# Optimization experiments

Hardware: AMD Instinct MI355X
Metric: run time of the kernel (lower is better)

Reference implementation:

```python
import jax, jax.numpy as jnp
import numpy as np

NUM_HEADS = 8
NUM_LAYERS = 4
TOKEN_AMOUNT = 16
TOKEN_SIZE = 256
D_MODEL = 512
D_FF = 2048


def _layernorm(x, g, b, eps=1e-6):
    m = jnp.mean(x, axis=-1, keepdims=True)
    v = jnp.mean((x - m) ** 2, axis=-1, keepdims=True)
    return (x - m) / jnp.sqrt(v + eps) * g + b


def _mha(xq, xkv, W, b, mask, H):
    # W: [4, d, d] (q,k,v,o), b: [4, d]
    B, Tq, d = xq.shape
    Tk = xkv.shape[1]
    dh = d // H
    q = (xq @ W[0] + b[0]).reshape(B, Tq, H, dh).transpose(0, 2, 1, 3)
    k = (xkv @ W[1] + b[1]).reshape(B, Tk, H, dh).transpose(0, 2, 1, 3)
    v = (xkv @ W[2] + b[2]).reshape(B, Tk, H, dh).transpose(0, 2, 1, 3)
    logits = jnp.einsum('bhqd,bhkd->bhqk', q, k) / jnp.sqrt(jnp.float32(dh))
    if mask is not None:
        logits = logits - mask * jnp.finfo(jnp.float32).max
    w = jax.nn.softmax(logits, axis=-1)
    o = jnp.einsum('bhqk,bhkd->bhqd', w, v).transpose(0, 2, 1, 3).reshape(B, Tq, d)
    return o @ W[3] + b[3]


def _pos_enc(T, d):
    i = jnp.arange(d)
    factors = 1.0 / jnp.power(10000.0, (2.0 * (i // 2)).astype(jnp.float32) / d)
    ang = jnp.arange(T, dtype=jnp.float32)[:, None] * factors  # [T, d]
    return jnp.where(i % 2 == 0, jnp.sin(ang), jnp.cos(ang))


def setup_inputs() -> dict:
    key = jax.random.key(0)
    ks = jax.random.split(key, 8)
    B, Lenc, F = 16, 2048, 128
    d, dff, L, TS = D_MODEL, D_FF, NUM_LAYERS, TOKEN_SIZE
    s = 0.02
    return {
        'encoder_output': jax.random.normal(ks[0], (B, Lenc, d), jnp.float32),
        'encoder_input': jax.random.normal(ks[1], (B, Lenc, F), jnp.float32),
        'emb_W': jax.random.normal(ks[2], (TS, d), jnp.float32) * s,
        'emb_b': jnp.zeros((d,), jnp.float32),
        'out_W': jax.random.normal(ks[3], (d, TS), jnp.float32) * s,
        'out_b': jnp.zeros((TS,), jnp.float32),
        'self_W': jax.random.normal(ks[4], (L, 4, d, d), jnp.float32) * s,
        'self_b': jnp.zeros((L, 4, d), jnp.float32),
        'cross_W': jax.random.normal(ks[5], (L, 4, d, d), jnp.float32) * s,
        'cross_b': jnp.zeros((L, 4, d), jnp.float32),
        'ffn_W1': jax.random.normal(ks[6], (L, d, dff), jnp.float32) * s,
        'ffn_b1': jnp.zeros((L, dff), jnp.float32),
        'ffn_W2': jax.random.normal(ks[7], (L, dff, d), jnp.float32) * s,
        'ffn_b2': jnp.zeros((L, d), jnp.float32),
        'ln_g': jnp.ones((L, 3, d), jnp.float32),
        'ln_b': jnp.zeros((L, 3, d), jnp.float32),
    }


def reference(encoder_output, encoder_input, emb_W, emb_b, out_W, out_b,
              self_W, self_b, cross_W, cross_b,
              ffn_W1, ffn_b1, ffn_W2, ffn_b2, ln_g, ln_b):
    B = encoder_output.shape[0]
    d = emb_W.shape[1]
    H = NUM_HEADS
    # padding mask from encoder_input (mask_zero_inputs=True)
    pad_mask = jnp.min((encoder_input == 0).astype(jnp.float32), axis=2)[:, None, None, :]
    tokens = jnp.ones((B, 1, TOKEN_SIZE), dtype=jnp.float32)
    for _ in range(TOKEN_AMOUNT):
        T = tokens.shape[1]
        look_ahead = 1.0 - jnp.tril(jnp.ones((T, T), dtype=jnp.float32))
        tok_pad = jnp.min((tokens == 0).astype(jnp.float32), axis=2)[:, None, None, :]
        la_mask = jnp.maximum(tok_pad, look_ahead)
        x = (tokens @ emb_W + emb_b) * jnp.sqrt(jnp.float32(d)) + _pos_enc(T, d)
        for l in range(NUM_LAYERS):
            a = _mha(x, x, self_W[l], self_b[l], la_mask, H)
            x = _layernorm(x + a, ln_g[l, 0], ln_b[l, 0])
            c = _mha(x, encoder_output, cross_W[l], cross_b[l], pad_mask, H)
            x = _layernorm(x + c, ln_g[l, 1], ln_b[l, 1])
            f = jax.nn.relu(x @ ffn_W1[l] + ffn_b1[l]) @ ffn_W2[l] + ffn_b2[l]
            x = _layernorm(x + f, ln_g[l, 2], ln_b[l, 2])
        next_token = (x @ out_W + out_b)[:, -1:, :]
        tokens = jnp.concatenate([tokens, next_token], axis=1)
    return tokens[:, 1:, :]
```

## Files before the change

### kernel.cpp

```cpp
#include <hip/hip_runtime.h>


typedef unsigned short ushort_t;
typedef __attribute__((ext_vector_type(4))) float f32x4;
typedef __attribute__((ext_vector_type(8))) unsigned short us8;
typedef __attribute__((ext_vector_type(4))) unsigned short us4;

#define NB 256
#define NTHR 1024

__device__ __forceinline__ float bf2f(ushort_t u) {
    union { unsigned int i; float f; } v; v.i = ((unsigned int)u) << 16; return v.f;
}
__device__ __forceinline__ ushort_t f2bf(float f) {
    union { unsigned int i; float f; } v; v.f = f;
    return (ushort_t)((v.i + 0x7FFF + ((v.i >> 16) & 1)) >> 16);
}
__device__ __forceinline__ float wave_sum(float v) {
    #pragma unroll
    for (int m = 32; m; m >>= 1) v += __shfl_xor(v, m);
    return v;
}
__device__ __forceinline__ float wave_max(float v) {
    #pragma unroll
    for (int m = 32; m; m >>= 1) v = fmaxf(v, __shfl_xor(v, m));
    return v;
}

union U64C { unsigned long long u; float2 f; };
__device__ __forceinline__ float clf(const float* p) {
    return __hip_atomic_load(p, __ATOMIC_RELAXED, __HIP_MEMORY_SCOPE_AGENT);
}
__device__ __forceinline__ void csf(float* p, float v) {
    __hip_atomic_store(p, v, __ATOMIC_RELAXED, __HIP_MEMORY_SCOPE_AGENT);
}
__device__ __forceinline__ float2 clf2(const float* p) {
    U64C c; c.u = __hip_atomic_load((unsigned long long*)p, __ATOMIC_RELAXED,
                                    __HIP_MEMORY_SCOPE_AGENT);
    return c.f;
}
__device__ __forceinline__ void csf2(float* p, float x, float y) {
    U64C c; c.f.x = x; c.f.y = y;
    __hip_atomic_store((unsigned long long*)p, c.u, __ATOMIC_RELAXED,
                       __HIP_MEMORY_SCOPE_AGENT);
}

__device__ __forceinline__ void gbar(unsigned* bar, int g) {
    __syncthreads();
    if (threadIdx.x == 0) {
        unsigned* cnt = bar + g * 32;
        unsigned* rel = bar + 512 + g * 32;
        unsigned a = __hip_atomic_fetch_add(cnt, 1u, __ATOMIC_RELAXED,
                                            __HIP_MEMORY_SCOPE_AGENT);
        unsigned e = (a >> 4) + 1u;
        if ((a & 15u) == 15u) {
            __hip_atomic_store(rel, e, __ATOMIC_RELAXED, __HIP_MEMORY_SCOPE_AGENT);
        } else {
            while ((int)(__hip_atomic_load(rel, __ATOMIC_RELAXED,
                                           __HIP_MEMORY_SCOPE_AGENT) - e) < 0)
                __builtin_amdgcn_s_sleep(1);
        }
    }
    __syncthreads();
}

__device__ __forceinline__ void ln512b(const float* __restrict__ row,
                                       const float* __restrict__ g,
                                       const float* __restrict__ be,
                                       int use_ln, float* dst, float* red) {
    int tid = threadIdx.x;
    float a = (tid < 512) ? clf(row + tid) : 0.f;
    if (use_ln) {
        float s = a, s2 = a * a;
        #pragma unroll
        for (int m = 32; m; m >>= 1) {
            s  += __shfl_xor(s, m);
            s2 += __shfl_xor(s2, m);
        }
        if ((tid & 63) == 0) { red[tid >> 6] = s; red[16 + (tid >> 6)] = s2; }
        __syncthreads();
        float ts = 0.f, ts2 = 0.f;
        #pragma unroll
        for (int i = 0; i < 8; i++) { ts += red[i]; ts2 += red[16 + i]; }
        float mu = ts * (1.f / 512.f);
        float var = ts2 * (1.f / 512.f) - mu * mu;
        float rstd = rsqrtf(var + 1e-6f);
        if (tid < 512) dst[tid] = (a - mu) * rstd * g[tid] + be[tid];
    } else {
        if (tid < 512) dst[tid] = a;
    }
    __syncthreads();
}

template<int NCQ, int K>
__device__ __forceinline__ void gemv_all(const float* xs, const float* __restrict__ W,
                                         int ldw, int col0, float* part) {
    constexpr int S = 1024 / NCQ;
    constexpr int KS = K / S;
    int tid = threadIdx.x;
    int cq = tid & (NCQ - 1), ks = tid / NCQ;
    const float* Wp = W + (size_t)(ks * KS) * ldw + col0 + cq * 4;
    const float* xp = xs + ks * KS;
    f32x4 acc = {0.f, 0.f, 0.f, 0.f};
    #pragma unroll
    for (int r = 0; r < KS; r++)
        acc += xp[r] * *(const f32x4*)(Wp + (size_t)r * ldw);
    #pragma unroll
    for (int m = NCQ; m < 64; m <<= 1) {
        acc[0] += __shfl_xor(acc[0], m);
        acc[1] += __shfl_xor(acc[1], m);
        acc[2] += __shfl_xor(acc[2], m);
        acc[3] += __shfl_xor(acc[3], m);
    }
    int wave = tid >> 6, lane = tid & 63;
    if (lane < NCQ) *(f32x4*)(part + (wave * NCQ + lane) * 4) = acc;
    __syncthreads();
}
template<int NCQ>
__device__ __forceinline__ float gemv_allr(const float* part) {
    float a = 0.f;
    #pragma unroll
    for (int w = 0; w < 16; w++) a += part[w * NCQ * 4 + threadIdx.x];
    return a;
}

struct Args {
    const float *enc, *encIn, *embW, *embB, *outW, *outB;
    const float *selfW, *selfB, *crossW, *crossB;
    const float *fW1, *fb1, *fW2, *fb2, *lng, *lnb;
    float* out;
    unsigned* bar;
    float *x0, *qbuf, *y1, *y2, *y3, *attnb;
    float *lny1, *lny2, *qt, *Pm2, *Ps2, *Pz, *tmpb, *selfK, *selfV;
};


__global__ __launch_bounds__(NTHR, 4) void k_mega(Args A) {
    __shared__ ushort_t encL[128 * 520];
    __shared__ float padL[128];
    __shared__ float sm[6400];
    const int bid = blockIdx.x, tid = threadIdx.x;
    const int b = bid >> 4, r = bid & 15;
    unsigned* bar = A.bar;

    {
        const float* ep = A.enc + ((size_t)b * 2048 + r * 128) * 512;
        #pragma unroll 4
        for (int it = 0; it < 16; it++) {
            int idx = tid + it * 1024;
            int key = idx >> 7;
            int d = (idx & 127) * 4;
            float4 v = *(const float4*)(ep + (size_t)key * 512 + d);
            us4 o; o[0] = f2bf(v.x); o[1] = f2bf(v.y); o[2] = f2bf(v.z); o[3] = f2bf(v.w);
            *(us4*)(encL + key * 520 + d) = o;
        }
        int key = tid >> 3, sub = tid & 7;
        const float* p = A.encIn + ((size_t)b * 2048 + r * 128 + key) * 128 + sub * 16;
        int ok = 1;
        #pragma unroll
        for (int j = 0; j < 4; j++) {
            float4 v = *(const float4*)(p + j * 4);
            ok &= (v.x == 0.f) & (v.y == 0.f) & (v.z == 0.f) & (v.w == 0.f);
        }
        ok &= __shfl_xor(ok, 1); ok &= __shfl_xor(ok, 2); ok &= __shfl_xor(ok, 4);
        if (sub == 0) padL[key] = ok ? 1.f : 0.f;
    }
    __syncthreads();

    for (int t = 0; t < 16; t++) {
        {
            float* tok = sm;
            float* part = sm + 256;
            if (tid < 256)
                tok[tid] = (t == 0) ? 1.f
                         : clf(A.out + (size_t)b * 4096 + (t - 1) * 256 + tid);
            __syncthreads();
            gemv_all<8, 256>(tok, A.embW, 512, r * 32, part);
            if (tid < 32) {
                float acc = gemv_allr<8>(part);
                int col = r * 32 + tid;
                float expo = (2.0f * (float)(col >> 1)) * (1.f / 512.f);
                float ang = (float)t * powf(10000.0f, -expo);
                float pv = (col & 1) ? cosf(ang) : sinf(ang);
                csf(A.x0 + (size_t)b * 512 + col,
                    (acc + A.embB[col]) * 22.627416997969522f + pv);
            }
        }
        gbar(bar, b);

        for (int l = 0; l < 4; l++) {
            const float* src = (l == 0) ? A.x0 : A.y3;
            const float* gP = (l == 0) ? nullptr : A.lng + ((l - 1) * 3 + 2) * 512;
            const float* bP = (l == 0) ? nullptr : A.lnb + ((l - 1) * 3 + 2) * 512;
            int ulnP = (l != 0);

            {
                float* xs = sm;
                float* red = sm + 512;
                float* part = sm + 1024;
                ln512b(src + (size_t)b * 512, gP, bP, ulnP, xs, red);
                int cq = tid & 7, ks = tid >> 3;
                const float* xp = xs + ks * 4;
                f32x4 a0 = {0.f,0.f,0.f,0.f}, a1 = a0, a2 = a0;
                const float* W0 = A.selfW + ((size_t)(l * 4 + 0)) * 262144
                                + (size_t)(ks * 4) * 512 + r * 32 + cq * 4;
                const float* W1 = W0 + 262144;
                const float* W2 = W1 + 262144;
                #pragma unroll
                for (int rr = 0; rr < 4; rr++) {
                    float x = xp[rr];
                    a0 += x * *(const f32x4*)(W0 + (size_t)rr * 512);
                    a1 += x * *(const f32x4*)(W1 + (size_t)rr * 512);
                    a2 += x * *(const f32x4*)(W2 + (size_t)rr * 512);
                }
                #pragma unroll
                for (int m = 8; m < 64; m <<= 1) {
                    #pragma unroll
                    for (int j = 0; j < 4; j++) {
                        a0[j] += __shfl_xor(a0[j], m);
                        a1[j] += __shfl_xor(a1[j], m);
                        a2[j] += __shfl_xor(a2[j], m);
                    }
                }
                int wave = tid >> 6, lane = tid & 63;
                if (lane < 8) {
                    *(f32x4*)(part + (wave * 8 + lane) * 4) = a0;
                    *(f32x4*)(part + 512 + (wave * 8 + lane) * 4) = a1;
                    *(f32x4*)(part + 1024 + (wave * 8 + lane) * 4) = a2;
                }
                __syncthreads();
                if (tid < 96) {
                    int m = tid >> 5, j = tid & 31;
                    float a = 0.f;
                    #pragma unroll
                    for (int w = 0; w < 16; w++) a += part[m * 512 + w * 32 + j];
                    int col = r * 32 + j;
                    a += A.selfB[(l * 4 + m) * 512 + col];
                    if (m == 0) csf(A.qbuf + (size_t)b * 512 + col, a);
                    else if (m == 1)
                        csf(A.selfK + (((size_t)l * 16 + b) * 16 + t) * 512 + col, a);
                    else
                        csf(A.selfV + (((size_t)l * 16 + b) * 16 + t) * 512 + col, a);
                }
            }
            gbar(bar, b);

            {
                float* xr = sm;
                float* qs = sm + 512;
                float* as2 = sm + 1024;
                float* lg = sm + 2048;
                float* red = sm + 2176;
                float* part = sm + 2560;
                ln512b(src + (size_t)b * 512, gP, bP, ulnP, xr, red);
                if (tid < 256) {
                    float2 v = clf2(A.qbuf + (size_t)b * 512 + tid * 2);
                    qs[tid * 2] = v.x; qs[tid * 2 + 1] = v.y;
                }
                __syncthreads();
                const float* Kb = A.selfK + ((size_t)l * 16 + b) * 16 * 512;
                const float* Vb = A.selfV + ((size_t)l * 16 + b) * 16 * 512;
                if (tid < 512) {
                    int idx = tid >> 2, q4 = tid & 3;
                    int h = idx >> 4, j = idx & 15;
                    if (j <= t) {
                        const float* kp = Kb + (size_t)j * 512 + h * 64 + q4 * 16;
                        const float* qp = qs + h * 64 + q4 * 16;
                        float s = 0.f;
                        #pragma unroll
                        for (int d = 0; d < 16; d += 2) {
                            float2 kv = clf2(kp + d);
                            s += qp[d] * kv.x + qp[d + 1] * kv.y;
                        }
                        s += __shfl_xor(s, 1);
                        s += __shfl_xor(s, 2);
                        if (q4 == 0) lg[h * 16 + j] = s * 0.125f;
                    }
                }
                __syncthreads();
                if (tid < 8) {
                    float m = -1e30f;
                    for (int j = 0; j <= t; j++) m = fmaxf(m, lg[tid * 16 + j]);
                    float ssum = 0.f;
                    for (int j = 0; j <= t; j++) {
                        float e = __expf(lg[tid * 16 + j] - m);
                        lg[tid * 16 + j] = e; ssum += e;
                    }
                    float inv = 1.f / ssum;
                    for (int j = 0; j <= t; j++) lg[tid * 16 + j] *= inv;
                }
                __syncthreads();
                {
                    int col = tid & 511, jh = tid >> 9;
                    float a = 0.f;
                    for (int j = jh; j <= t; j += 2)
                        a += lg[(col >> 6) * 16 + j] * clf(Vb + (size_t)j * 512 + col);
                    as2[jh * 512 + col] = a;
                }
                __syncthreads();
                if (tid < 512) qs[tid] = as2[tid] + as2[512 + tid];
                __syncthreads();
                gemv_all<8, 512>(qs, A.selfW + ((size_t)(l * 4 + 3)) * 262144,
                                 512, r * 32, part);
                if (tid < 32) {
                    int col = r * 32 + tid;
                    csf(A.y1 + (size_t)b * 512 + col,
                        gemv_allr<8>(part) + A.selfB[(l * 4 + 3) * 512 + col] + xr[col]);
                }
            }
            gbar(bar, b);

            {
                int h = r >> 1, half = r & 1;
                float* xsw = sm;
                float* red = sm + 512;
                float* qch = sm + 544;
                float* part = sm + 1024;
                ln512b(A.y1 + (size_t)b * 512, A.lng + (l * 3) * 512,
                       A.lnb + (l * 3) * 512, 1, xsw, red);
                if (r == 0 && tid < 512)
                    csf(A.lny1 + (size_t)b * 512 + tid, xsw[tid]);
                gemv_all<16, 512>(xsw, A.crossW + ((size_t)(l * 4)) * 262144,
                                  512, h * 64, part);
                if (tid < 64)
                    qch[tid] = gemv_allr<16>(part)
                             + A.crossB[(l * 4) * 512 + h * 64 + tid];
                __syncthreads();
                {
                    int D = half * 256 + (tid >> 2), q4 = tid & 3;
                    const float* wr = A.crossW + ((size_t)(l * 4 + 1)) * 262144
                                    + (size_t)D * 512 + h * 64 + q4 * 16;
                    const float* qp = qch + q4 * 16;
                    float a = 0.f;
                    #pragma unroll
                    for (int j = 0; j < 16; j += 4) {
                        f32x4 wv = *(const f32x4*)(wr + j);
                        a += qp[j]*wv[0] + qp[j+1]*wv[1] + qp[j+2]*wv[2] + qp[j+3]*wv[3];
                    }
                    a += __shfl_xor(a, 1);
                    a += __shfl_xor(a, 2);
                    if (q4 == 0)
                        csf(A.qt + ((size_t)b * 8 + h) * 512 + D, a * 0.125f);
                }
            }
            gbar(bar, b);

            {
                float* qts = sm;
                float* lge = sm + 4160;
                float* wms = sm + 5184;
                float* wss = sm + 5200;
                #pragma unroll
                for (int it = 0; it < 2; it++) {
                    int p = (tid + it * 1024) * 2;
                    float2 v = clf2(A.qt + (size_t)b * 4096 + p);
                    int row = p >> 9, d = p & 511;
                    qts[row * 520 + d] = v.x;
                    qts[row * 520 + d + 1] = v.y;
                }
                __syncthreads();
                #pragma unroll
                for (int it = 0; it < 4; it++) {
                    int key = it * 32 + (tid >> 5);
                    int hh = (tid >> 2) & 7, pq = tid & 3;
                    const ushort_t* er = encL + key * 520;
                    const float* q = qts + hh * 520;
                    float a0 = 0.f, a1 = 0.f;
                    #pragma unroll
                    for (int ch = 0; ch < 16; ch++) {
                        int c8 = (pq + ch * 4) * 8;
                        us8 ev8 = *(const us8*)(er + c8);
                        const float* qp = q + c8;
                        a0 += bf2f(ev8[0])*qp[0] + bf2f(ev8[1])*qp[1]
                            + bf2f(ev8[2])*qp[2] + bf2f(ev8[3])*qp[3];
                        a1 += bf2f(ev8[4])*qp[4] + bf2f(ev8[5])*qp[5]
                            + bf2f(ev8[6])*qp[6] + bf2f(ev8[7])*qp[7];
                    }
                    float acc = a0 + a1;
                    acc += __shfl_xor(acc, 1);
                    acc += __shfl_xor(acc, 2);
                    if (pq == 0)
                        lge[hh * 128 + key] = (padL[key] != 0.f) ? -2e30f : acc;
                }
                __syncthreads();
                {
                    int hh = tid >> 7, k = tid & 127;
                    float lv = lge[hh * 128 + k];
                    float mv = wave_max(lv);
                    if ((tid & 63) == 0) wms[tid >> 6] = mv;
                    __syncthreads();
                    float m = fmaxf(wms[hh * 2], wms[hh * 2 + 1]);
                    float ev = __expf(lv - m);
                    float sv = wave_sum(ev);
                    if ((tid & 63) == 0) wss[tid >> 6] = sv;
                    lge[hh * 128 + k] = ev;
                    __syncthreads();
                    if (tid < 8) {
                        int bc = b * 16 + r;
                        csf(A.Pm2 + bc * 8 + tid, fmaxf(wms[tid * 2], wms[tid * 2 + 1]));
                        csf(A.Ps2 + bc * 8 + tid, wss[tid * 2] + wss[tid * 2 + 1]);
                    }
                }
                __syncthreads();
                {
                    int hz = tid >> 7, ii = tid & 127;
                    f32x4 z = {0.f, 0.f, 0.f, 0.f};
                    const ushort_t* ep2 = encL + ii * 4;
                    const float* le = lge + hz * 128;
                    #pragma unroll 4
                    for (int k = 0; k < 128; k++) {
                        float ev = le[k];
                        us4 e4 = *(const us4*)(ep2 + k * 520);
                        z[0] += ev * bf2f(e4[0]); z[1] += ev * bf2f(e4[1]);
                        z[2] += ev * bf2f(e4[2]); z[3] += ev * bf2f(e4[3]);
                    }
                    float* dst = A.Pz + ((size_t)((b * 16 + r) * 8 + hz)) * 512 + ii * 4;
                    csf2(dst, z[0], z[1]);
                    csf2(dst + 2, z[2], z[3]);
                }
            }
            gbar(bar, b);

            {
                int h = r >> 1, half = r & 1;
                float* zs = sm;
                float* zs2 = sm + 512;
                float* ecs = sm + 2560;
                float* part = sm + 2624;
                if (tid < 16) {
                    float mcv = clf(A.Pm2 + (b * 16 + tid) * 8 + h);
                    float mm = mcv;
                    mm = fmaxf(mm, __shfl_xor(mm, 1));
                    mm = fmaxf(mm, __shfl_xor(mm, 2));
                    mm = fmaxf(mm, __shfl_xor(mm, 4));
                    mm = fmaxf(mm, __shfl_xor(mm, 8));
                    float ec = __expf(mcv - mm);
                    float sv = ec * clf(A.Ps2 + (b * 16 + tid) * 8 + h);
                    sv += __shfl_xor(sv, 1); sv += __shfl_xor(sv, 2);
                    sv += __shfl_xor(sv, 4); sv += __shfl_xor(sv, 8);
                    ecs[tid] = ec;
                    if (tid == 0) ecs[16] = 1.f / sv;
                }
                __syncthreads();
                {
                    int cp = (tid & 255) * 2, qtr = tid >> 8;
                    float a0 = 0.f, a1 = 0.f;
                    #pragma unroll
                    for (int j = 0; j < 4; j++) {
                        int cc = qtr * 4 + j;
                        float2 v = clf2(A.Pz + ((size_t)(b * 16 + cc) * 8 + h) * 512 + cp);
                        a0 += ecs[cc] * v.x; a1 += ecs[cc] * v.y;
                    }
                    zs2[qtr * 512 + cp] = a0;
                    zs2[qtr * 512 + cp + 1] = a1;
                }
                __syncthreads();
                if (tid < 512)
                    zs[tid] = (zs2[tid] + zs2[512 + tid] + zs2[1024 + tid]
                             + zs2[1536 + tid]) * ecs[16];
                __syncthreads();
                gemv_all<8, 512>(zs, A.crossW + ((size_t)(l * 4 + 2)) * 262144,
                                 512, h * 64 + half * 32, part);
                if (tid < 32) {
                    int col = h * 64 + half * 32 + tid;
                    csf(A.attnb + (size_t)b * 512 + col,
                        gemv_allr<8>(part) + A.crossB[(l * 4 + 2) * 512 + col]);
                }
            }
            gbar(bar, b);

            {
                float* xa = sm;
                float* part = sm + 512;
                if (tid < 256) {
                    float2 v = clf2(A.attnb + (size_t)b * 512 + tid * 2);
                    xa[tid * 2] = v.x; xa[tid * 2 + 1] = v.y;
                }
                __syncthreads();
                gemv_all<8, 512>(xa, A.crossW + ((size_t)(l * 4 + 3)) * 262144,
                                 512, r * 32, part);
                if (tid < 32) {
                    int col = r * 32 + tid;
                    csf(A.y2 + (size_t)b * 512 + col,
                        gemv_allr<8>(part) + A.crossB[(l * 4 + 3) * 512 + col]
                        + clf(A.lny1 + (size_t)b * 512 + col));
                }
            }
            gbar(bar, b);

            {
                float* xsw = sm;
                float* red = sm + 512;
                float* part = sm + 1024;
                ln512b(A.y2 + (size_t)b * 512, A.lng + (l * 3 + 1) * 512,
                       A.lnb + (l * 3 + 1) * 512, 1, xsw, red);
                if (r == 0 && tid < 512)
                    csf(A.lny2 + (size_t)b * 512 + tid, xsw[tid]);
                gemv_all<32, 512>(xsw, A.fW1 + (size_t)l * 512 * 2048,
                                  2048, r * 128, part);
                if (tid < 128) {
                    int col = r * 128 + tid;
                    csf(A.tmpb + (size_t)b * 2048 + col,
                        fmaxf(gemv_allr<32>(part) + A.fb1[l * 2048 + col], 0.f));
                }
            }
            gbar(bar, b);

            {
                float* ts = sm;
                float* part = sm + 2048;
                {
                    float2 v = clf2(A.tmpb + (size_t)b * 2048 + tid * 2);
                    ts[tid * 2] = v.x; ts[tid * 2 + 1] = v.y;
                }
                __syncthreads();
                gemv_all<8, 2048>(ts, A.fW2 + (size_t)l * 2048 * 512,
                                  512, r * 32, part);
                if (tid < 32) {
                    int col = r * 32 + tid;
                    csf(A.y3 + (size_t)b * 512 + col,
                        gemv_allr<8>(part) + A.fb2[l * 512 + col]
                        + clf(A.lny2 + (size_t)b * 512 + col));
                }
            }
            gbar(bar, b);
        }

        {
            float* xsw = sm;
            float* red = sm + 512;
            float* part = sm + 1024;
            ln512b(A.y3 + (size_t)b * 512, A.lng + 11 * 512, A.lnb + 11 * 512,
                   1, xsw, red);
            gemv_all<4, 512>(xsw, A.outW, 256, r * 16, part);
            if (tid < 16) {
                int col = r * 16 + tid;
                csf(A.out + (size_t)b * 4096 + t * 256 + col,
                    gemv_allr<4>(part) + A.outB[col]);
            }
        }
        gbar(bar, b);
    }
}


extern "C" void kernel_launch(void* const* d_in, const int* in_sizes, int n_in,
                              void* d_out, int out_size, void* d_ws, size_t ws_size,
                              hipStream_t stream) {
    Args A;
    A.enc    = (const float*)d_in[0];
    A.encIn  = (const float*)d_in[1];
    A.embW   = (const float*)d_in[2];
    A.embB   = (const float*)d_in[3];
    A.outW   = (const float*)d_in[4];
    A.outB   = (const float*)d_in[5];
    A.selfW  = (const float*)d_in[6];
    A.selfB  = (const float*)d_in[7];
    A.crossW = (const float*)d_in[8];
    A.crossB = (const float*)d_in[9];
    A.fW1    = (const float*)d_in[10];
    A.fb1    = (const float*)d_in[11];
    A.fW2    = (const float*)d_in[12];
    A.fb2    = (const float*)d_in[13];
    A.lng    = (const float*)d_in[14];
    A.lnb    = (const float*)d_in[15];
    A.out    = (float*)d_out;

    char* ws = (char*)d_ws;
    size_t off = 0;
    auto alloc = [&](size_t bytes) -> char* {
        char* p = ws + off;
        off = (off + bytes + 255) & ~(size_t)255;
        return p;
    };
    char* barrier = alloc(4096);
    A.bar = (unsigned*)barrier;
    A.x0    = (float*)alloc(16 * 512 * 4);
    A.qbuf  = (float*)alloc(16 * 512 * 4);
    A.y1    = (float*)alloc(16 * 512 * 4);
    A.y2    = (float*)alloc(16 * 512 * 4);
    A.y3    = (float*)alloc(16 * 512 * 4);
    A.attnb = (float*)alloc(16 * 512 * 4);
    A.lny1  = (float*)alloc(16 * 512 * 4);
    A.lny2  = (float*)alloc(16 * 512 * 4);
    A.qt    = (float*)alloc((size_t)16 * 8 * 512 * 4);
    A.Pm2   = (float*)alloc(16 * 16 * 8 * 4);
    A.Ps2   = (float*)alloc(16 * 16 * 8 * 4);
    A.Pz    = (float*)alloc((size_t)16 * 16 * 8 * 512 * 4);
    A.tmpb  = (float*)alloc((size_t)16 * 2048 * 4);
    A.selfK = (float*)alloc((size_t)4 * 16 * 16 * 512 * 4);
    A.selfV = (float*)alloc((size_t)4 * 16 * 16 * 512 * 4);
    if (off > ws_size) return;

    hipMemsetAsync(barrier, 0, 4096, stream);
    k_mega<<<dim3(NB), dim3(NTHR), 0, stream>>>(A);
}
```

Baseline: 4.997 ms.

## Convert layer weights to bf16 once per launch and stream bf16 in GEMVs

At kernel start every block converts a slice of the self, cross and FFN weight matrices from fp32 to bf16 in workspace, then a new grid-wide barrier makes the copies visible to all blocks. All later per-token GEMVs read bf16 weights and widen them to fp32 in registers, halving the weight bytes streamed on each of the 16 decode steps. The cost is a one-time conversion pass and one global barrier, plus reduced weight precision that could move outputs relative to the fp32 reference.

```diff
diff --git a/kernel.cpp b/kernel.cpp
--- a/kernel.cpp
+++ b/kernel.cpp
@@ -16,6 +16,9 @@
     union { unsigned int i; float f; } v; v.f = f;
     return (ushort_t)((v.i + 0x7FFF + ((v.i >> 16) & 1)) >> 16);
 }
+__device__ __forceinline__ f32x4 b2f4(us4 w) {
+    return (f32x4){bf2f(w[0]), bf2f(w[1]), bf2f(w[2]), bf2f(w[3])};
+}
 __device__ __forceinline__ float wave_sum(float v) {
     #pragma unroll
     for (int m = 32; m; m >>= 1) v += __shfl_xor(v, m);
@@ -27,7 +30,7 @@
     return v;
 }
 
-union U64C { unsigned long long u; float2 f; };
+union U64C { unsigned long long u; float2 f; us4 s4; };
 __device__ __forceinline__ float clf(const float* p) {
     return __hip_atomic_load(p, __ATOMIC_RELAXED, __HIP_MEMORY_SCOPE_AGENT);
 }
@@ -41,6 +44,11 @@
 }
 __device__ __forceinline__ void csf2(float* p, float x, float y) {
     U64C c; c.f.x = x; c.f.y = y;
+    __hip_atomic_store((unsigned long long*)p, c.u, __ATOMIC_RELAXED,
+                       __HIP_MEMORY_SCOPE_AGENT);
+}
+__device__ __forceinline__ void csu4(ushort_t* p, us4 v) {
+    U64C c; c.s4 = v;
     __hip_atomic_store((unsigned long long*)p, c.u, __ATOMIC_RELAXED,
                        __HIP_MEMORY_SCOPE_AGENT);
 }
@@ -64,6 +72,25 @@
     __syncthreads();
 }
 
+__device__ __forceinline__ void gbar_all(unsigned* bar) {
+    __syncthreads();
+    if (threadIdx.x == 0) {
+        unsigned* cnt = bar + 1024;
+        unsigned* rel = bar + 1056;
+        unsigned a = __hip_atomic_fetch_add(cnt, 1u, __ATOMIC_RELAXED,
+                                            __HIP_MEMORY_SCOPE_AGENT);
+        unsigned e = (a >> 8) + 1u;
+        if ((a & 255u) == 255u) {
+            __hip_atomic_store(rel, e, __ATOMIC_RELAXED, __HIP_MEMORY_SCOPE_AGENT);
+        } else {
+            while ((int)(__hip_atomic_load(rel, __ATOMIC_RELAXED,
+                                           __HIP_MEMORY_SCOPE_AGENT) - e) < 0)
+                __builtin_amdgcn_s_sleep(1);
+        }
+    }
+    __syncthreads();
+}
+
 __device__ __forceinline__ void ln512b(const float* __restrict__ row,
                                        const float* __restrict__ g,
                                        const float* __restrict__ be,
@@ -93,8 +120,8 @@
 }
 
 template<int NCQ, int K>
-__device__ __forceinline__ void gemv_all(const float* xs, const float* __restrict__ W,
-                                         int ldw, int col0, float* part) {
+__device__ __forceinline__ void gemv_allf(const float* xs, const float* __restrict__ W,
+                                          int ldw, int col0, float* part) {
     constexpr int S = 1024 / NCQ;
     constexpr int KS = K / S;
     int tid = threadIdx.x;
@@ -116,6 +143,31 @@
     if (lane < NCQ) *(f32x4*)(part + (wave * NCQ + lane) * 4) = acc;
     __syncthreads();
 }
+
+template<int NCQ, int K>
+__device__ __forceinline__ void gemv_allb(const float* xs, const ushort_t* __restrict__ W,
+                                          int ldw, int col0, float* part) {
+    constexpr int S = 1024 / NCQ;
+    constexpr int KS = K / S;
+    int tid = threadIdx.x;
+    int cq = tid & (NCQ - 1), ks = tid / NCQ;
+    const ushort_t* Wp = W + (size_t)(ks * KS) * ldw + col0 + cq * 4;
+    const float* xp = xs + ks * KS;
+    f32x4 acc = {0.f, 0.f, 0.f, 0.f};
+    #pragma unroll
+    for (int r = 0; r < KS; r++)
+        acc += xp[r] * b2f4(*(const us4*)(Wp + (size_t)r * ldw));
+    #pragma unroll
+    for (int m = NCQ; m < 64; m <<= 1) {
+        acc[0] += __shfl_xor(acc[0], m);
+        acc[1] += __shfl_xor(acc[1], m);
+        acc[2] += __shfl_xor(acc[2], m);
+        acc[3] += __shfl_xor(acc[3], m);
+    }
+    int wave = tid >> 6, lane = tid & 63;
+    if (lane < NCQ) *(f32x4*)(part + (wave * NCQ + lane) * 4) = acc;
+    __syncthreads();
+}
 template<int NCQ>
 __device__ __forceinline__ float gemv_allr(const float* part) {
     float a = 0.f;
@@ -132,6 +184,7 @@
     unsigned* bar;
     float *x0, *qbuf, *y1, *y2, *y3, *attnb;
     float *lny1, *lny2, *qt, *Pm2, *Ps2, *Pz, *tmpb, *selfK, *selfV;
+    ushort_t *selfWb, *crossWb, *fW1b, *fW2b;
 };
 
 
@@ -164,8 +217,22 @@
         }
         ok &= __shfl_xor(ok, 1); ok &= __shfl_xor(ok, 2); ok &= __shfl_xor(ok, 4);
         if (sub == 0) padL[key] = ok ? 1.f : 0.f;
+        const float* srcs[4] = {A.selfW, A.crossW, A.fW1, A.fW2};
+        ushort_t* dsts[4] = {A.selfWb, A.crossWb, A.fW1b, A.fW2b};
+        #pragma unroll
+        for (int a = 0; a < 4; a++) {
+            const float* s = srcs[a];
+            ushort_t* d = dsts[a];
+            #pragma unroll
+            for (int it = 0; it < 4; it++) {
+                size_t i = (size_t)bid * 16384 + (size_t)(it * 1024 + tid) * 4;
+                float4 v = *(const float4*)(s + i);
+                us4 o; o[0] = f2bf(v.x); o[1] = f2bf(v.y); o[2] = f2bf(v.z); o[3] = f2bf(v.w);
+                csu4(d + i, o);
+            }
+        }
     }
-    __syncthreads();
+    gbar_all(bar);
 
     for (int t = 0; t < 16; t++) {
         {
@@ -175,7 +242,7 @@
                 tok[tid] = (t == 0) ? 1.f
                          : clf(A.out + (size_t)b * 4096 + (t - 1) * 256 + tid);
             __syncthreads();
-            gemv_all<8, 256>(tok, A.embW, 512, r * 32, part);
+            gemv_allf<8, 256>(tok, A.embW, 512, r * 32, part);
             if (tid < 32) {
                 float acc = gemv_allr<8>(part);
                 int col = r * 32 + tid;
@@ -202,16 +269,16 @@
                 int cq = tid & 7, ks = tid >> 3;
                 const float* xp = xs + ks * 4;
                 f32x4 a0 = {0.f,0.f,0.f,0.f}, a1 = a0, a2 = a0;
-                const float* W0 = A.selfW + ((size_t)(l * 4 + 0)) * 262144
-                                + (size_t)(ks * 4) * 512 + r * 32 + cq * 4;
-                const float* W1 = W0 + 262144;
-                const float* W2 = W1 + 262144;
+                const ushort_t* W0 = A.selfWb + ((size_t)(l * 4 + 0)) * 262144
+                                   + (size_t)(ks * 4) * 512 + r * 32 + cq * 4;
+                const ushort_t* W1 = W0 + 262144;
+                const ushort_t* W2 = W1 + 262144;
                 #pragma unroll
                 for (int rr = 0; rr < 4; rr++) {
                     float x = xp[rr];
-                    a0 += x * *(const f32x4*)(W0 + (size_t)rr * 512);
-                    a1 += x * *(const f32x4*)(W1 + (size_t)rr * 512);
-                    a2 += x * *(const f32x4*)(W2 + (size_t)rr * 512);
+                    a0 += x * b2f4(*(const us4*)(W0 + (size_t)rr * 512));
+                    a1 += x * b2f4(*(const us4*)(W1 + (size_t)rr * 512));
+                    a2 += x * b2f4(*(const us4*)(W2 + (size_t)rr * 512));
                 }
                 #pragma unroll
                 for (int m = 8; m < 64; m <<= 1) {
@@ -300,8 +367,8 @@
                 __syncthreads();
                 if (tid < 512) qs[tid] = as2[tid] + as2[512 + tid];
                 __syncthreads();
-                gemv_all<8, 512>(qs, A.selfW + ((size_t)(l * 4 + 3)) * 262144,
-                                 512, r * 32, part);
+                gemv_allb<8, 512>(qs, A.selfWb + ((size_t)(l * 4 + 3)) * 262144,
+                                  512, r * 32, part);
                 if (tid < 32) {
                     int col = r * 32 + tid;
                     csf(A.y1 + (size_t)b * 512 + col,
@@ -320,21 +387,21 @@
                        A.lnb + (l * 3) * 512, 1, xsw, red);
                 if (r == 0 && tid < 512)
                     csf(A.lny1 + (size_t)b * 512 + tid, xsw[tid]);
-                gemv_all<16, 512>(xsw, A.crossW + ((size_t)(l * 4)) * 262144,
-                                  512, h * 64, part);
+                gemv_allb<16, 512>(xsw, A.crossWb + ((size_t)(l * 4)) * 262144,
+                                   512, h * 64, part);
                 if (tid < 64)
                     qch[tid] = gemv_allr<16>(part)
                              + A.crossB[(l * 4) * 512 + h * 64 + tid];
                 __syncthreads();
                 {
                     int D = half * 256 + (tid >> 2), q4 = tid & 3;
-                    const float* wr = A.crossW + ((size_t)(l * 4 + 1)) * 262144
-                                    + (size_t)D * 512 + h * 64 + q4 * 16;
+                    const ushort_t* wr = A.crossWb + ((size_t)(l * 4 + 1)) * 262144
+                                       + (size_t)D * 512 + h * 64 + q4 * 16;
                     const float* qp = qch + q4 * 16;
                     float a = 0.f;
                     #pragma unroll
                     for (int j = 0; j < 16; j += 4) {
-                        f32x4 wv = *(const f32x4*)(wr + j);
+                        f32x4 wv = b2f4(*(const us4*)(wr + j));
                         a += qp[j]*wv[0] + qp[j+1]*wv[1] + qp[j+2]*wv[2] + qp[j+3]*wv[3];
                     }
                     a += __shfl_xor(a, 1);
@@ -459,8 +526,8 @@
                     zs[tid] = (zs2[tid] + zs2[512 + tid] + zs2[1024 + tid]
                              + zs2[1536 + tid]) * ecs[16];
                 __syncthreads();
-                gemv_all<8, 512>(zs, A.crossW + ((size_t)(l * 4 + 2)) * 262144,
-                                 512, h * 64 + half * 32, part);
+                gemv_allb<8, 512>(zs, A.crossWb + ((size_t)(l * 4 + 2)) * 262144,
+                                  512, h * 64 + half * 32, part);
                 if (tid < 32) {
                     int col = h * 64 + half * 32 + tid;
                     csf(A.attnb + (size_t)b * 512 + col,
@@ -477,8 +544,8 @@
                     xa[tid * 2] = v.x; xa[tid * 2 + 1] = v.y;
                 }
                 __syncthreads();
-                gemv_all<8, 512>(xa, A.crossW + ((size_t)(l * 4 + 3)) * 262144,
-                                 512, r * 32, part);
+                gemv_allb<8, 512>(xa, A.crossWb + ((size_t)(l * 4 + 3)) * 262144,
+                                  512, r * 32, part);
                 if (tid < 32) {
                     int col = r * 32 + tid;
                     csf(A.y2 + (size_t)b * 512 + col,
@@ -496,8 +563,8 @@
                        A.lnb + (l * 3 + 1) * 512, 1, xsw, red);
                 if (r == 0 && tid < 512)
                     csf(A.lny2 + (size_t)b * 512 + tid, xsw[tid]);
-                gemv_all<32, 512>(xsw, A.fW1 + (size_t)l * 512 * 2048,
-                                  2048, r * 128, part);
+                gemv_allb<32, 512>(xsw, A.fW1b + (size_t)l * 512 * 2048,
+                                   2048, r * 128, part);
                 if (tid < 128) {
                     int col = r * 128 + tid;
                     csf(A.tmpb + (size_t)b * 2048 + col,
@@ -514,8 +581,8 @@
                     ts[tid * 2] = v.x; ts[tid * 2 + 1] = v.y;
                 }
                 __syncthreads();
-                gemv_all<8, 2048>(ts, A.fW2 + (size_t)l * 2048 * 512,
-                                  512, r * 32, part);
+                gemv_allb<8, 2048>(ts, A.fW2b + (size_t)l * 2048 * 512,
+                                   512, r * 32, part);
                 if (tid < 32) {
                     int col = r * 32 + tid;
                     csf(A.y3 + (size_t)b * 512 + col,
@@ -532,7 +599,7 @@
             float* part = sm + 1024;
             ln512b(A.y3 + (size_t)b * 512, A.lng + 11 * 512, A.lnb + 11 * 512,
                    1, xsw, red);
-            gemv_all<4, 512>(xsw, A.outW, 256, r * 16, part);
+            gemv_allf<4, 512>(xsw, A.outW, 256, r * 16, part);
             if (tid < 16) {
                 int col = r * 16 + tid;
                 csf(A.out + (size_t)b * 4096 + t * 256 + col,
@@ -573,7 +640,7 @@
         off = (off + bytes + 255) & ~(size_t)255;
         return p;
     };
-    char* barrier = alloc(4096);
+    char* barrier = alloc(8192);
     A.bar = (unsigned*)barrier;
     A.x0    = (float*)alloc(16 * 512 * 4);
     A.qbuf  = (float*)alloc(16 * 512 * 4);
@@ -590,8 +657,12 @@
     A.tmpb  = (float*)alloc((size_t)16 * 2048 * 4);
     A.selfK = (float*)alloc((size_t)4 * 16 * 16 * 512 * 4);
     A.selfV = (float*)alloc((size_t)4 * 16 * 16 * 512 * 4);
+    A.selfWb  = (ushort_t*)alloc((size_t)4 * 4 * 512 * 512 * 2);
+    A.crossWb = (ushort_t*)alloc((size_t)4 * 4 * 512 * 512 * 2);
+    A.fW1b    = (ushort_t*)alloc((size_t)4 * 512 * 2048 * 2);
+    A.fW2b    = (ushort_t*)alloc((size_t)4 * 2048 * 512 * 2);
     if (off > ws_size) return;
 
-    hipMemsetAsync(barrier, 0, 4096, stream);
+    hipMemsetAsync(barrier, 0, 8192, stream);
     k_mega<<<dim3(NB), dim3(NTHR), 0, stream>>>(A);
 }
```

After: 4.860 ms. 1.03x faster.
